# Kernel optimization log

Measured on AMD Instinct MI355X. Metric: run time of the kernel, lower is better.

The kernel has to match this reference:

```python
import jax, jax.numpy as jnp
import numpy as np

B, K, D = 16384, 32, 64
N_USERS, N_ENT, N_REL = 100000, 100000, 32
MAX_NORM = 1.0


def renorm(e):
    # emulate torch nn.Embedding(max_norm=1): rescale rows with norm > 1
    n = jnp.linalg.norm(e, axis=-1, keepdims=True)
    return e * jnp.minimum(1.0, MAX_NORM / jnp.maximum(n, 1e-7))


def setup_inputs() -> dict:
    key = jax.random.key(0)
    ks = jax.random.split(key, 9)
    return {
        "user_table": jax.random.normal(ks[0], (N_USERS, D), dtype=jnp.float32),
        "entity_table": jax.random.normal(ks[1], (N_ENT, D), dtype=jnp.float32),
        "relation_table": jax.random.normal(ks[2], (N_REL, D), dtype=jnp.float32),
        "W": jax.random.normal(ks[3], (D, D), dtype=jnp.float32) / np.sqrt(D),
        "b": jnp.zeros((D,), dtype=jnp.float32),
        "users": jax.random.randint(ks[4], (B,), 0, N_USERS),
        "items": jax.random.randint(ks[5], (B,), 0, N_ENT),
        "adj_entity": jax.random.randint(ks[6], (N_ENT, K), 0, N_ENT),
        "adj_relation": jax.random.randint(ks[7], (N_ENT, K), 0, N_REL),
    }


def reference(user_table, entity_table, relation_table, W, b,
              users, items, adj_entity, adj_relation):
    # neighbor id gather: [B, K]
    nbr_ent_ids = adj_entity[items]
    nbr_rel_ids = adj_relation[items]
    # embedding lookups with max_norm renorm
    user_emb = renorm(user_table[users])                 # [B, D]
    item_emb = renorm(entity_table[items])               # [B, D]
    nbr_ent = renorm(entity_table[nbr_ent_ids])          # [B, K, D]
    nbr_rel = renorm(relation_table[nbr_rel_ids])        # [B, K, D]
    # user-relation attention scores, softmax over neighbors
    scores = jnp.einsum('bd,bkd->bk', user_emb, nbr_rel)  # [B, K]
    attn = jax.nn.softmax(scores, axis=-1)
    # attention-weighted neighbor aggregation
    nbr_vec = jnp.einsum('bk,bkd->bd', attn, nbr_ent)     # [B, D]
    # sum aggregator + linear + relu (dropout omitted: eval-mode baseline)
    out = item_emb + nbr_vec
    out = jax.nn.relu(out @ W.T + b)
    return (user_emb, out)
```

## Files before the change

### kernel.cpp

```cpp
#include <hip/hip_runtime.h>
#include <math.h>

#define BB 16384
#define KK_N 32
#define DD 64
#define N_ENT 100000
#define N_REL 32

#define WS_REL_OFF_BYTES ((size_t)N_ENT * DD * 2)
#define WS_NEED_BYTES (WS_REL_OFF_BYTES + (size_t)N_REL * DD * 4)

#define PT_ENT  N_ENT
#define PT_USER (N_ENT + BB)
#define PT_ALL  (N_ENT + BB + N_REL)

typedef _Float16 f16x8 __attribute__((ext_vector_type(8)));
typedef _Float16 f16x4 __attribute__((ext_vector_type(4)));
typedef float    f32x4 __attribute__((ext_vector_type(4)));

__device__ __forceinline__ float dot4(float4 a, float4 b) {
    return a.x * b.x + a.y * b.y + a.z * b.z + a.w * b.w;
}
__device__ __forceinline__ float red16(float ss) {
    ss += __shfl_xor(ss, 1, 64);
    ss += __shfl_xor(ss, 2, 64);
    ss += __shfl_xor(ss, 4, 64);
    ss += __shfl_xor(ss, 8, 64);
    return ss;
}
__device__ __forceinline__ unsigned short f2bf(float x) {
    unsigned int u = __float_as_uint(x);
    u += 0x7fffu + ((u >> 16) & 1u);
    return (unsigned short)(u >> 16);
}
__device__ __forceinline__ float bf2f(unsigned short h) {
    return __uint_as_float(((unsigned int)h) << 16);
}
__device__ __forceinline__ float4 bf4(ushort4 h) {
    return make_float4(bf2f(h.x), bf2f(h.y), bf2f(h.z), bf2f(h.w));
}

__global__ __launch_bounds__(256) void precompute(
    const float* __restrict__ user_table,
    const float* __restrict__ entity_table,
    const float* __restrict__ relation_table,
    const int*   __restrict__ users,
    unsigned short* __restrict__ ent_bf,
    float* __restrict__ rel_ws,
    float* __restrict__ out_user)
{
    const int tid = threadIdx.x;
    const int gl  = tid & 15;
    const int t   = blockIdx.x * 16 + (tid >> 4);
    if (t >= PT_ALL) return;

    if (t < PT_ENT) {
        float4 v = *reinterpret_cast<const float4*>(&entity_table[(size_t)t * DD + gl * 4]);
        float ss = red16(dot4(v, v));
        float sc = fminf(1.0f, __builtin_amdgcn_rsqf(ss));
        ushort4 h;
        h.x = f2bf(v.x * sc); h.y = f2bf(v.y * sc);
        h.z = f2bf(v.z * sc); h.w = f2bf(v.w * sc);
        *reinterpret_cast<ushort4*>(&ent_bf[(size_t)t * DD + gl * 4]) = h;
    } else if (t < PT_USER) {
        int u = t - PT_ENT;
        int uid = users[u];
        float4 v = *reinterpret_cast<const float4*>(&user_table[(size_t)uid * DD + gl * 4]);
        float ss = red16(dot4(v, v));
        float sc = fminf(1.0f, __builtin_amdgcn_rsqf(ss));
        v.x *= sc; v.y *= sc; v.z *= sc; v.w *= sc;
        *reinterpret_cast<float4*>(&out_user[(size_t)u * DD + gl * 4]) = v;
    } else {
        int rr = t - PT_USER;
        float4 v = *reinterpret_cast<const float4*>(&relation_table[rr * DD + gl * 4]);
        float ss = red16(dot4(v, v));
        float sc = fminf(1.0f, __builtin_amdgcn_rsqf(ss));
        v.x *= sc; v.y *= sc; v.z *= sc; v.w *= sc;
        *reinterpret_cast<float4*>(&rel_ws[rr * DD + ((gl * 4) ^ ((rr & 15) << 2))]) = v;
    }
}

__global__ __launch_bounds__(256) void kgcn_main(
    const unsigned short* __restrict__ ent_bf,
    const float* __restrict__ rel_ws,
    const float* __restrict__ W,
    const float* __restrict__ bias,
    const int*   __restrict__ items,
    const int*   __restrict__ adj_entity,
    const int*   __restrict__ adj_relation,
    const float* __restrict__ user_out,
    float* __restrict__ out_final)
{
    __shared__ __align__(16) float RelLds[N_REL * DD];
    __shared__ __align__(16) float Uv[4][2][64];
    __shared__ __align__(16) _Float16 Th[16][72];

    const int tid  = threadIdx.x;
    const int lane = tid & 63;
    const int wave = tid >> 6;
    const int grp  = lane >> 4;
    const int gl   = lane & 15;
    const int kk   = lane & 31;

    const int b0 = (blockIdx.x * 4 + wave) * 2;
    const int iid0 = __builtin_amdgcn_readfirstlane(items[b0]);
    const int iid1 = __builtin_amdgcn_readfirstlane(items[b0 + 1]);

    const int* abase = (lane < 32) ? adj_entity : adj_relation;
    const int adjv0 = abase[(size_t)iid0 * KK_N + kk];
    const int adjv1 = abase[(size_t)iid1 * KK_N + kk];

    int eid0[8], eid1[8];
    #pragma unroll
    for (int k0 = 0; k0 < 8; ++k0) {
        eid0[k0] = adj_entity[(size_t)iid0 * KK_N + k0 * 4 + grp];
        eid1[k0] = adj_entity[(size_t)iid1 * KK_N + k0 * 4 + grp];
    }
    ushort4 v0[8], v1[8];
    #pragma unroll
    for (int k0 = 0; k0 < 8; ++k0) {
        v0[k0] = *reinterpret_cast<const ushort4*>(&ent_bf[(size_t)eid0[k0] * DD + gl * 4]);
        v1[k0] = *reinterpret_cast<const ushort4*>(&ent_bf[(size_t)eid1[k0] * DD + gl * 4]);
    }
    float4 uv0 = *reinterpret_cast<const float4*>(&user_out[(size_t)b0 * DD + gl * 4]);
    float4 uv1 = *reinterpret_cast<const float4*>(&user_out[(size_t)(b0 + 1) * DD + gl * 4]);
    ushort4 it0 = *reinterpret_cast<const ushort4*>(&ent_bf[(size_t)iid0 * DD + gl * 4]);
    ushort4 it1 = *reinterpret_cast<const ushort4*>(&ent_bf[(size_t)iid1 * DD + gl * 4]);

    #pragma unroll
    for (int it = 0; it < 2; ++it)
        reinterpret_cast<float4*>(RelLds)[tid + it * 256] =
            reinterpret_cast<const float4*>(rel_ws)[tid + it * 256];
    __syncthreads();

    if (lane < 16) {
        *reinterpret_cast<float4*>(&Uv[wave][0][gl * 4]) = uv0;
        *reinterpret_cast<float4*>(&Uv[wave][1][gl * 4]) = uv1;
    }

    const int rid0 = __shfl(adjv0, 32 + kk, 64);
    const int rid1 = __shfl(adjv1, 32 + kk, 64);
    const int sz0 = (rid0 & 15) << 2;
    const int sz1 = (rid1 & 15) << 2;
    const int dbase = (lane >> 5) * 32;
    float s0 = 0.0f, s1 = 0.0f;
    #pragma unroll
    for (int d0 = 0; d0 < 32; d0 += 4) {
        int d = dbase + d0;
        float4 q0 = *reinterpret_cast<const float4*>(&Uv[wave][0][d]);
        float4 r0 = *reinterpret_cast<const float4*>(&RelLds[rid0 * DD + (d ^ sz0)]);
        s0 += dot4(q0, r0);
        float4 q1 = *reinterpret_cast<const float4*>(&Uv[wave][1][d]);
        float4 r1 = *reinterpret_cast<const float4*>(&RelLds[rid1 * DD + (d ^ sz1)]);
        s1 += dot4(q1, r1);
    }
    s0 += __shfl_xor(s0, 32, 64);
    s1 += __shfl_xor(s1, 32, 64);

    float e0 = __expf(s0), e1 = __expf(s1);
    float sum0 = e0, sum1 = e1;
    #pragma unroll
    for (int m = 1; m < 32; m <<= 1) {
        sum0 += __shfl_xor(sum0, m, 64);
        sum1 += __shfl_xor(sum1, m, 64);
    }
    const float wk0 = e0 * __builtin_amdgcn_rcpf(sum0);
    const float wk1 = e1 * __builtin_amdgcn_rcpf(sum1);

    float4 acc0 = make_float4(0.f, 0.f, 0.f, 0.f);
    float4 acc1 = make_float4(0.f, 0.f, 0.f, 0.f);
    #pragma unroll
    for (int k0 = 0; k0 < 8; ++k0) {
        float c0 = __shfl(wk0, k0 * 4 + grp, 64);
        float4 f0 = bf4(v0[k0]);
        acc0.x = fmaf(c0, f0.x, acc0.x);
        acc0.y = fmaf(c0, f0.y, acc0.y);
        acc0.z = fmaf(c0, f0.z, acc0.z);
        acc0.w = fmaf(c0, f0.w, acc0.w);
        float c1 = __shfl(wk1, k0 * 4 + grp, 64);
        float4 f1 = bf4(v1[k0]);
        acc1.x = fmaf(c1, f1.x, acc1.x);
        acc1.y = fmaf(c1, f1.y, acc1.y);
        acc1.z = fmaf(c1, f1.z, acc1.z);
        acc1.w = fmaf(c1, f1.w, acc1.w);
    }
    #pragma unroll
    for (int m = 16; m < 64; m <<= 1) {
        acc0.x += __shfl_xor(acc0.x, m, 64);
        acc0.y += __shfl_xor(acc0.y, m, 64);
        acc0.z += __shfl_xor(acc0.z, m, 64);
        acc0.w += __shfl_xor(acc0.w, m, 64);
        acc1.x += __shfl_xor(acc1.x, m, 64);
        acc1.y += __shfl_xor(acc1.y, m, 64);
        acc1.z += __shfl_xor(acc1.z, m, 64);
        acc1.w += __shfl_xor(acc1.w, m, 64);
    }

    if (lane < 16) {
        float4 f0 = bf4(it0), f1 = bf4(it1);
        f16x4 h0, h1;
        h0[0] = (_Float16)(f0.x + acc0.x);
        h0[1] = (_Float16)(f0.y + acc0.y);
        h0[2] = (_Float16)(f0.z + acc0.z);
        h0[3] = (_Float16)(f0.w + acc0.w);
        h1[0] = (_Float16)(f1.x + acc1.x);
        h1[1] = (_Float16)(f1.y + acc1.y);
        h1[2] = (_Float16)(f1.z + acc1.z);
        h1[3] = (_Float16)(f1.w + acc1.w);
        *reinterpret_cast<f16x4*>(&Th[wave * 2 + 0][gl * 4]) = h0;
        *reinterpret_cast<f16x4*>(&Th[wave * 2 + 1][gl * 4]) = h1;
    }
    __syncthreads();

    const int n0  = wave * 16;
    const int row = lane & 15;
    const int kg  = (lane >> 4) * 8;
    f32x4 d = {0.f, 0.f, 0.f, 0.f};
    #pragma unroll
    for (int kb = 0; kb < 64; kb += 32) {
        f16x8 a = *reinterpret_cast<const f16x8*>(&Th[row][kb + kg]);
        const float* wr = &W[(size_t)(n0 + row) * DD + kb + kg];
        float4 w0 = *reinterpret_cast<const float4*>(wr);
        float4 w1 = *reinterpret_cast<const float4*>(wr + 4);
        f16x8 bfr;
        bfr[0] = (_Float16)w0.x; bfr[1] = (_Float16)w0.y;
        bfr[2] = (_Float16)w0.z; bfr[3] = (_Float16)w0.w;
        bfr[4] = (_Float16)w1.x; bfr[5] = (_Float16)w1.y;
        bfr[6] = (_Float16)w1.z; bfr[7] = (_Float16)w1.w;
        d = __builtin_amdgcn_mfma_f32_16x16x32_f16(a, bfr, d, 0, 0, 0);
    }
    const float bcol = bias[n0 + row];
    if (lane < 32) {
        #pragma unroll
        for (int r = 0; r < 4; ++r) {
            int orow = (lane >> 4) * 4 + r;
            int gb = blockIdx.x * 8 + orow;
            out_final[(size_t)gb * DD + n0 + row] = fmaxf(d[r] + bcol, 0.0f);
        }
    }
}

__global__ __launch_bounds__(256) void kgcn_fused(
    const float* __restrict__ user_table,
    const float* __restrict__ entity_table,
    const float* __restrict__ relation_table,
    const float* __restrict__ W,
    const float* __restrict__ bias,
    const int*   __restrict__ users,
    const int*   __restrict__ items,
    const int*   __restrict__ adj_entity,
    const int*   __restrict__ adj_relation,
    float* __restrict__ out_user,
    float* __restrict__ out_final)
{
    __shared__ __align__(16) float Wlds[64 * 64];
    __shared__ __align__(16) float RelLds[N_REL * DD];
    __shared__ __align__(16) float Vec[4][64];

    const int tid  = threadIdx.x;
    const int lane = tid & 63;
    const int wave = tid >> 6;
    const int grp  = lane >> 4;
    const int gl   = lane & 15;

    const int b = blockIdx.x * 4 + wave;
    const int uid = __builtin_amdgcn_readfirstlane(users[b]);
    const int iid = __builtin_amdgcn_readfirstlane(items[b]);

    const int kk = lane & 31;
    const int* abase = (lane < 32) ? adj_entity : adj_relation;
    const int adjv = abase[(size_t)iid * KK_N + kk];
    float4 uv = *reinterpret_cast<const float4*>(&user_table[(size_t)uid * DD + gl * 4]);
    float4 iv = *reinterpret_cast<const float4*>(&entity_table[(size_t)iid * DD + gl * 4]);

    #pragma unroll
    for (int it = 0; it < 4; ++it) {
        int i = tid + it * 256;
        float4 w4 = reinterpret_cast<const float4*>(W)[i];
        int d = i >> 4;
        int j = (i & 15) * 4;
        *reinterpret_cast<float4*>(&Wlds[d * 64 + (j ^ ((d & 15) << 2))]) = w4;
    }
    #pragma unroll
    for (int it = 0; it < 2; ++it) {
        int r = wave * 8 + it * 4 + grp;
        float4 vv = reinterpret_cast<const float4*>(relation_table)[r * 16 + gl];
        float ss = red16(dot4(vv, vv));
        float sc = fminf(1.0f, __builtin_amdgcn_rsqf(ss));
        vv.x *= sc; vv.y *= sc; vv.z *= sc; vv.w *= sc;
        *reinterpret_cast<float4*>(&RelLds[r * 64 + ((gl * 4) ^ ((r & 15) << 2))]) = vv;
    }

    float ssu = red16(dot4(uv, uv));
    float usc = fminf(1.0f, __builtin_amdgcn_rsqf(ssu));
    uv.x *= usc; uv.y *= usc; uv.z *= usc; uv.w *= usc;
    if (lane < 16)
        *reinterpret_cast<float4*>(&out_user[(size_t)b * DD + gl * 4]) = uv;

    int eid[8];
    #pragma unroll
    for (int k0 = 0; k0 < 8; ++k0)
        eid[k0] = __shfl(adjv, k0 * 4 + grp, 64);
    float4 v[8];
    #pragma unroll
    for (int k0 = 0; k0 < 8; ++k0)
        v[k0] = *reinterpret_cast<const float4*>(&entity_table[(size_t)eid[k0] * DD + gl * 4]);

    __syncthreads();
    if (lane < 16)
        *reinterpret_cast<float4*>(&Vec[wave][gl * 4]) = uv;

    const int rid = __shfl(adjv, 32 + kk, 64);
    const int srel = (rid & 15) << 2;
    const float* relrow = &RelLds[rid * 64];
    const int dbase = (lane >> 5) * 32;
    float score = 0.0f;
    #pragma unroll
    for (int d0 = 0; d0 < 32; d0 += 4) {
        int d = dbase + d0;
        float4 rv = *reinterpret_cast<const float4*>(&relrow[d ^ srel]);
        float4 tv = *reinterpret_cast<const float4*>(&Vec[wave][d]);
        score += dot4(tv, rv);
    }
    score += __shfl_xor(score, 32, 64);

    float mx = score;
    #pragma unroll
    for (int m = 1; m < 32; m <<= 1) mx = fmaxf(mx, __shfl_xor(mx, m, 64));
    float e = __expf(score - mx);
    float sum = e;
    #pragma unroll
    for (int m = 1; m < 32; m <<= 1) sum += __shfl_xor(sum, m, 64);
    const float attn = e * __builtin_amdgcn_rcpf(sum);

    float cc[8];
    #pragma unroll
    for (int k0 = 0; k0 < 8; ++k0)
        cc[k0] = __shfl(attn, k0 * 4 + grp, 64);

    float4 acc = make_float4(0.f, 0.f, 0.f, 0.f);
    #pragma unroll
    for (int k0 = 0; k0 < 8; ++k0) {
        float ss = red16(dot4(v[k0], v[k0]));
        float sc = fminf(1.0f, __builtin_amdgcn_rsqf(ss));
        float ck = cc[k0] * sc;
        acc.x = fmaf(ck, v[k0].x, acc.x);
        acc.y = fmaf(ck, v[k0].y, acc.y);
        acc.z = fmaf(ck, v[k0].z, acc.z);
        acc.w = fmaf(ck, v[k0].w, acc.w);
    }
    #pragma unroll
    for (int m = 16; m < 64; m <<= 1) {
        acc.x += __shfl_xor(acc.x, m, 64);
        acc.y += __shfl_xor(acc.y, m, 64);
        acc.z += __shfl_xor(acc.z, m, 64);
        acc.w += __shfl_xor(acc.w, m, 64);
    }

    float ssi = red16(dot4(iv, iv));
    float isc = fminf(1.0f, __builtin_amdgcn_rsqf(ssi));
    float4 tmp;
    tmp.x = fmaf(isc, iv.x, acc.x);
    tmp.y = fmaf(isc, iv.y, acc.y);
    tmp.z = fmaf(isc, iv.z, acc.z);
    tmp.w = fmaf(isc, iv.w, acc.w);
    if (lane < 16)
        *reinterpret_cast<float4*>(&Vec[wave][gl * 4]) = tmp;

    const float bv = bias[lane];
    const float* wrow = &Wlds[lane * 64];
    const int twz = (lane & 15) << 2;
    float o = bv;
    #pragma unroll
    for (int j0 = 0; j0 < 64; j0 += 4) {
        float4 wv = *reinterpret_cast<const float4*>(&wrow[j0 ^ twz]);
        float4 tv = *reinterpret_cast<const float4*>(&Vec[wave][j0]);
        o += dot4(tv, wv);
    }
    out_final[(size_t)b * DD + lane] = fmaxf(o, 0.0f);
}

extern "C" void kernel_launch(void* const* d_in, const int* in_sizes, int n_in,
                              void* d_out, int out_size, void* d_ws, size_t ws_size,
                              hipStream_t stream)
{
    const float* user_table     = (const float*)d_in[0];
    const float* entity_table   = (const float*)d_in[1];
    const float* relation_table = (const float*)d_in[2];
    const float* W              = (const float*)d_in[3];
    const float* bias           = (const float*)d_in[4];
    const int*   users          = (const int*)d_in[5];
    const int*   items          = (const int*)d_in[6];
    const int*   adj_entity     = (const int*)d_in[7];
    const int*   adj_relation   = (const int*)d_in[8];

    float* out_user  = (float*)d_out;
    float* out_final = (float*)d_out + (size_t)BB * DD;

    if (ws_size >= WS_NEED_BYTES) {
        unsigned short* ent_bf = (unsigned short*)d_ws;
        float* rel_ws = (float*)((char*)d_ws + WS_REL_OFF_BYTES);
        precompute<<<(PT_ALL + 15) / 16, 256, 0, stream>>>(
            user_table, entity_table, relation_table, users, ent_bf, rel_ws, out_user);
        kgcn_main<<<BB / 8, 256, 0, stream>>>(
            ent_bf, rel_ws, W, bias, items, adj_entity, adj_relation, out_user, out_final);
    } else {
        kgcn_fused<<<BB / 4, 256, 0, stream>>>(user_table, entity_table, relation_table,
                                               W, bias, users, items, adj_entity, adj_relation,
                                               out_user, out_final);
    }
}
```

Measured before the change: 30.65 us.

## Fuse precompute and main kernels into one cooperative persistent kernel with grid sync

Replaces the two-launch sequence (precompute renorm/bf16 conversion, then main gather-attention-MFMA kernel) with a single cooperative kernel. A persistent grid first renormalizes the entity and user tables, then synchronizes the whole grid before running the per-batch attention and linear layer. Each block also recomputes the relation table into LDS instead of reading it from workspace. This removes one kernel launch and the gap between launches, at the cost of a grid-wide barrier, reduced occupancy from the larger LDS footprint, and extra host-side occupancy queries on every call.

Result: slower. 95.57 us (+211.8%).

```diff
diff --git a/kernel.cpp b/kernel.cpp
--- a/kernel.cpp
+++ b/kernel.cpp
@@ -1,5 +1,8 @@
 #include <hip/hip_runtime.h>
+#include <hip/hip_cooperative_groups.h>
 #include <math.h>
+
+namespace cg = cooperative_groups;
 
 #define BB 16384
 #define KK_N 32
@@ -13,6 +16,8 @@
 #define PT_ENT  N_ENT
 #define PT_USER (N_ENT + BB)
 #define PT_ALL  (N_ENT + BB + N_REL)
+#define NU1 ((N_ENT + BB) / 16)
+#define NWB2 (BB / 8)
 
 typedef _Float16 f16x8 __attribute__((ext_vector_type(8)));
 typedef _Float16 f16x4 __attribute__((ext_vector_type(4)));
@@ -38,6 +43,199 @@
 }
 __device__ __forceinline__ float4 bf4(ushort4 h) {
     return make_float4(bf2f(h.x), bf2f(h.y), bf2f(h.z), bf2f(h.w));
+}
+
+__global__ __launch_bounds__(256) void kgcn_coop(
+    const float* __restrict__ user_table,
+    const float* __restrict__ entity_table,
+    const float* __restrict__ relation_table,
+    const float* __restrict__ W,
+    const float* __restrict__ bias,
+    const int*   __restrict__ users,
+    const int*   __restrict__ items,
+    const int*   __restrict__ adj_entity,
+    const int*   __restrict__ adj_relation,
+    unsigned short* __restrict__ ent_bf,
+    float* __restrict__ out_user,
+    float* __restrict__ out_final)
+{
+    __shared__ __align__(16) float RelLds[N_REL * DD];
+    __shared__ __align__(16) float Uv[4][2][64];
+    __shared__ __align__(16) _Float16 Th[16][72];
+
+    const int tid  = threadIdx.x;
+    const int lane = tid & 63;
+    const int wave = tid >> 6;
+    const int grp  = lane >> 4;
+    const int gl   = lane & 15;
+    const int kk   = lane & 31;
+
+    #pragma unroll
+    for (int it = 0; it < 2; ++it) {
+        int r = wave * 8 + it * 4 + grp;
+        float4 vv = reinterpret_cast<const float4*>(relation_table)[r * 16 + gl];
+        float ss = red16(dot4(vv, vv));
+        float sc = fminf(1.0f, __builtin_amdgcn_rsqf(ss));
+        vv.x *= sc; vv.y *= sc; vv.z *= sc; vv.w *= sc;
+        *reinterpret_cast<float4*>(&RelLds[r * 64 + ((gl * 4) ^ ((r & 15) << 2))]) = vv;
+    }
+
+    for (int u = blockIdx.x; u < NU1; u += gridDim.x) {
+        int t = u * 16 + (tid >> 4);
+        if (t < PT_ENT) {
+            float4 v = *reinterpret_cast<const float4*>(&entity_table[(size_t)t * DD + gl * 4]);
+            float ss = red16(dot4(v, v));
+            float sc = fminf(1.0f, __builtin_amdgcn_rsqf(ss));
+            ushort4 h;
+            h.x = f2bf(v.x * sc); h.y = f2bf(v.y * sc);
+            h.z = f2bf(v.z * sc); h.w = f2bf(v.w * sc);
+            *reinterpret_cast<ushort4*>(&ent_bf[(size_t)t * DD + gl * 4]) = h;
+        } else {
+            int uu = t - PT_ENT;
+            int uid = users[uu];
+            float4 v = *reinterpret_cast<const float4*>(&user_table[(size_t)uid * DD + gl * 4]);
+            float ss = red16(dot4(v, v));
+            float sc = fminf(1.0f, __builtin_amdgcn_rsqf(ss));
+            v.x *= sc; v.y *= sc; v.z *= sc; v.w *= sc;
+            *reinterpret_cast<float4*>(&out_user[(size_t)uu * DD + gl * 4]) = v;
+        }
+    }
+
+    cg::this_grid().sync();
+
+    for (int wb = blockIdx.x; wb < NWB2; wb += gridDim.x) {
+        const int b0 = (wb * 4 + wave) * 2;
+        const int iid0 = __builtin_amdgcn_readfirstlane(items[b0]);
+        const int iid1 = __builtin_amdgcn_readfirstlane(items[b0 + 1]);
+
+        const int* abase = (lane < 32) ? adj_entity : adj_relation;
+        const int adjv0 = abase[(size_t)iid0 * KK_N + kk];
+        const int adjv1 = abase[(size_t)iid1 * KK_N + kk];
+
+        int eid0[8], eid1[8];
+        #pragma unroll
+        for (int k0 = 0; k0 < 8; ++k0) {
+            eid0[k0] = adj_entity[(size_t)iid0 * KK_N + k0 * 4 + grp];
+            eid1[k0] = adj_entity[(size_t)iid1 * KK_N + k0 * 4 + grp];
+        }
+        ushort4 v0[8], v1[8];
+        #pragma unroll
+        for (int k0 = 0; k0 < 8; ++k0) {
+            v0[k0] = *reinterpret_cast<const ushort4*>(&ent_bf[(size_t)eid0[k0] * DD + gl * 4]);
+            v1[k0] = *reinterpret_cast<const ushort4*>(&ent_bf[(size_t)eid1[k0] * DD + gl * 4]);
+        }
+        float4 uv0 = *reinterpret_cast<const float4*>(&out_user[(size_t)b0 * DD + gl * 4]);
+        float4 uv1 = *reinterpret_cast<const float4*>(&out_user[(size_t)(b0 + 1) * DD + gl * 4]);
+        ushort4 it0 = *reinterpret_cast<const ushort4*>(&ent_bf[(size_t)iid0 * DD + gl * 4]);
+        ushort4 it1 = *reinterpret_cast<const ushort4*>(&ent_bf[(size_t)iid1 * DD + gl * 4]);
+
+        if (lane < 16) {
+            *reinterpret_cast<float4*>(&Uv[wave][0][gl * 4]) = uv0;
+            *reinterpret_cast<float4*>(&Uv[wave][1][gl * 4]) = uv1;
+        }
+
+        const int rid0 = __shfl(adjv0, 32 + kk, 64);
+        const int rid1 = __shfl(adjv1, 32 + kk, 64);
+        const int sz0 = (rid0 & 15) << 2;
+        const int sz1 = (rid1 & 15) << 2;
+        const int dbase = (lane >> 5) * 32;
+        float s0 = 0.0f, s1 = 0.0f;
+        #pragma unroll
+        for (int d0 = 0; d0 < 32; d0 += 4) {
+            int d = dbase + d0;
+            float4 q0 = *reinterpret_cast<const float4*>(&Uv[wave][0][d]);
+            float4 r0 = *reinterpret_cast<const float4*>(&RelLds[rid0 * DD + (d ^ sz0)]);
+            s0 += dot4(q0, r0);
+            float4 q1 = *reinterpret_cast<const float4*>(&Uv[wave][1][d]);
+            float4 r1 = *reinterpret_cast<const float4*>(&RelLds[rid1 * DD + (d ^ sz1)]);
+            s1 += dot4(q1, r1);
+        }
+        s0 += __shfl_xor(s0, 32, 64);
+        s1 += __shfl_xor(s1, 32, 64);
+
+        float e0 = __expf(s0), e1 = __expf(s1);
+        float sum0 = e0, sum1 = e1;
+        #pragma unroll
+        for (int m = 1; m < 32; m <<= 1) {
+            sum0 += __shfl_xor(sum0, m, 64);
+            sum1 += __shfl_xor(sum1, m, 64);
+        }
+        const float wk0 = e0 * __builtin_amdgcn_rcpf(sum0);
+        const float wk1 = e1 * __builtin_amdgcn_rcpf(sum1);
+
+        float4 acc0 = make_float4(0.f, 0.f, 0.f, 0.f);
+        float4 acc1 = make_float4(0.f, 0.f, 0.f, 0.f);
+        #pragma unroll
+        for (int k0 = 0; k0 < 8; ++k0) {
+            float c0 = __shfl(wk0, k0 * 4 + grp, 64);
+            float4 f0 = bf4(v0[k0]);
+            acc0.x = fmaf(c0, f0.x, acc0.x);
+            acc0.y = fmaf(c0, f0.y, acc0.y);
+            acc0.z = fmaf(c0, f0.z, acc0.z);
+            acc0.w = fmaf(c0, f0.w, acc0.w);
+            float c1 = __shfl(wk1, k0 * 4 + grp, 64);
+            float4 f1 = bf4(v1[k0]);
+            acc1.x = fmaf(c1, f1.x, acc1.x);
+            acc1.y = fmaf(c1, f1.y, acc1.y);
+            acc1.z = fmaf(c1, f1.z, acc1.z);
+            acc1.w = fmaf(c1, f1.w, acc1.w);
+        }
+        #pragma unroll
+        for (int m = 16; m < 64; m <<= 1) {
+            acc0.x += __shfl_xor(acc0.x, m, 64);
+            acc0.y += __shfl_xor(acc0.y, m, 64);
+            acc0.z += __shfl_xor(acc0.z, m, 64);
+            acc0.w += __shfl_xor(acc0.w, m, 64);
+            acc1.x += __shfl_xor(acc1.x, m, 64);
+            acc1.y += __shfl_xor(acc1.y, m, 64);
+            acc1.z += __shfl_xor(acc1.z, m, 64);
+            acc1.w += __shfl_xor(acc1.w, m, 64);
+        }
+
+        __syncthreads();
+        if (lane < 16) {
+            float4 f0 = bf4(it0), f1 = bf4(it1);
+            f16x4 h0, h1;
+            h0[0] = (_Float16)(f0.x + acc0.x);
+            h0[1] = (_Float16)(f0.y + acc0.y);
+            h0[2] = (_Float16)(f0.z + acc0.z);
+            h0[3] = (_Float16)(f0.w + acc0.w);
+            h1[0] = (_Float16)(f1.x + acc1.x);
+            h1[1] = (_Float16)(f1.y + acc1.y);
+            h1[2] = (_Float16)(f1.z + acc1.z);
+            h1[3] = (_Float16)(f1.w + acc1.w);
+            *reinterpret_cast<f16x4*>(&Th[wave * 2 + 0][gl * 4]) = h0;
+            *reinterpret_cast<f16x4*>(&Th[wave * 2 + 1][gl * 4]) = h1;
+        }
+        __syncthreads();
+
+        const int n0  = wave * 16;
+        const int row = lane & 15;
+        const int kg  = (lane >> 4) * 8;
+        f32x4 d = {0.f, 0.f, 0.f, 0.f};
+        #pragma unroll
+        for (int kb = 0; kb < 64; kb += 32) {
+            f16x8 a = *reinterpret_cast<const f16x8*>(&Th[row][kb + kg]);
+            const float* wr = &W[(size_t)(n0 + row) * DD + kb + kg];
+            float4 w0 = *reinterpret_cast<const float4*>(wr);
+            float4 w1 = *reinterpret_cast<const float4*>(wr + 4);
+            f16x8 bfr;
+            bfr[0] = (_Float16)w0.x; bfr[1] = (_Float16)w0.y;
+            bfr[2] = (_Float16)w0.z; bfr[3] = (_Float16)w0.w;
+            bfr[4] = (_Float16)w1.x; bfr[5] = (_Float16)w1.y;
+            bfr[6] = (_Float16)w1.z; bfr[7] = (_Float16)w1.w;
+            d = __builtin_amdgcn_mfma_f32_16x16x32_f16(a, bfr, d, 0, 0, 0);
+        }
+        const float bcol = bias[n0 + row];
+        if (lane < 32) {
+            #pragma unroll
+            for (int r = 0; r < 4; ++r) {
+                int orow = (lane >> 4) * 4 + r;
+                int gb = wb * 8 + orow;
+                out_final[(size_t)gb * DD + n0 + row] = fmaxf(d[r] + bcol, 0.0f);
+            }
+        }
+    }
 }
 
 __global__ __launch_bounds__(256) void precompute(
@@ -400,10 +598,34 @@
     if (ws_size >= WS_NEED_BYTES) {
         unsigned short* ent_bf = (unsigned short*)d_ws;
         float* rel_ws = (float*)((char*)d_ws + WS_REL_OFF_BYTES);
-        precompute<<<(PT_ALL + 15) / 16, 256, 0, stream>>>(
-            user_table, entity_table, relation_table, users, ent_bf, rel_ws, out_user);
-        kgcn_main<<<BB / 8, 256, 0, stream>>>(
-            ent_bf, rel_ws, W, bias, items, adj_entity, adj_relation, out_user, out_final);
+
+        int dev = 0;
+        (void)hipGetDevice(&dev);
+        int ncu = 0;
+        (void)hipDeviceGetAttribute(&ncu, hipDeviceAttributeMultiprocessorCount, dev);
+        int maxb = 0;
+        hipError_t oe = hipOccupancyMaxActiveBlocksPerMultiprocessor(&maxb, kgcn_coop, 256, 0);
+        int grid = (oe == hipSuccess && ncu > 0) ? maxb * ncu : 0;
+        if (grid > NWB2) grid = NWB2;
+
+        bool done = false;
+        if (grid >= 64) {
+            void* kargs[] = {
+                (void*)&user_table, (void*)&entity_table, (void*)&relation_table,
+                (void*)&W, (void*)&bias, (void*)&users, (void*)&items,
+                (void*)&adj_entity, (void*)&adj_relation,
+                (void*)&ent_bf, (void*)&out_user, (void*)&out_final
+            };
+            hipError_t le = hipLaunchCooperativeKernel((void*)kgcn_coop, dim3(grid), dim3(256),
+                                                       kargs, 0, stream);
+            done = (le == hipSuccess);
+        }
+        if (!done) {
+            precompute<<<(PT_ALL + 15) / 16, 256, 0, stream>>>(
+                user_table, entity_table, relation_table, users, ent_bf, rel_ws, out_user);
+            kgcn_main<<<BB / 8, 256, 0, stream>>>(
+                ent_bf, rel_ws, W, bias, items, adj_entity, adj_relation, out_user, out_final);
+        }
     } else {
         kgcn_fused<<<BB / 4, 256, 0, stream>>>(user_table, entity_table, relation_table,
                                                W, bias, users, items, adj_entity, adj_relation,
```
